# Kernel tuning notes

Measured on AMD Instinct MI355X. Metric: run time of the kernel, lower is better.

The kernel has to match this reference:

```python
import jax, jax.numpy as jnp
import numpy as np

BN_EPS = 1e-5

def _conv1x1(x, w, b=None):
    # x: [B,C,H,W], w: [O,C] -> [B,O,H,W]
    y = jnp.einsum('bchw,oc->bohw', x, w)
    if b is not None:
        y = y + b[None, :, None, None]
    return y

def _bn_silu(y, gamma, beta):
    # BN inference with running_mean=0, running_var=1, then SiLU
    scale = gamma / jnp.sqrt(1.0 + BN_EPS)
    y = y * scale[None, :, None, None] + beta[None, :, None, None]
    return jax.nn.silu(y)

def setup_inputs() -> dict:
    key = jax.random.key(0)
    ks = jax.random.split(key, 20)
    B, D, S = 32, 512, 32
    C = D // 2
    d = {}
    d['x'] = jax.random.normal(ks[0], (B, D, S, S), jnp.float32)
    d['cv1_w'] = jax.random.normal(ks[1], (C, D), jnp.float32) * (1.0 / np.sqrt(D))
    d['cv1_gamma'] = jax.random.uniform(ks[2], (C,), jnp.float32, 0.5, 1.5)
    d['cv1_beta'] = jax.random.normal(ks[3], (C,), jnp.float32) * 0.1
    d['q_w'] = jax.random.normal(ks[4], (C, C), jnp.float32) * (1.0 / np.sqrt(C))
    d['q_b'] = jax.random.normal(ks[5], (C,), jnp.float32) * 0.02
    d['k_w'] = jax.random.normal(ks[6], (C, C), jnp.float32) * (1.0 / np.sqrt(C))
    d['k_b'] = jax.random.normal(ks[7], (C,), jnp.float32) * 0.02
    d['v_w'] = jax.random.normal(ks[8], (C, C), jnp.float32) * (1.0 / np.sqrt(C))
    d['v_b'] = jax.random.normal(ks[9], (C,), jnp.float32) * 0.02
    d['e_w'] = jax.random.normal(ks[10], (C, C), jnp.float32) * (1.0 / np.sqrt(C))
    d['e_b'] = jax.random.normal(ks[11], (C,), jnp.float32) * 0.02
    d['rel_h'] = jax.random.normal(ks[12], (1, C, S, 1), jnp.float32)
    d['rel_w'] = jax.random.normal(ks[13], (1, C, 1, S), jnp.float32)
    d['cv2_w'] = jax.random.normal(ks[14], (D, C), jnp.float32) * (1.0 / np.sqrt(C))
    d['cv2_gamma'] = jax.random.uniform(ks[15], (D,), jnp.float32, 0.5, 1.5)
    d['cv2_beta'] = jax.random.normal(ks[16], (D,), jnp.float32) * 0.1
    return d

def reference(x, cv1_w, cv1_gamma, cv1_beta, q_w, q_b, k_w, k_b, v_w, v_b,
              e_w, e_b, rel_h, rel_w, cv2_w, cv2_gamma, cv2_beta):
    # cv1: 1x1 conv (no bias) + BN + SiLU
    x1 = _bn_silu(_conv1x1(x, cv1_w), cv1_gamma, cv1_beta)  # [B,C,H,W]
    B, C, H, W = x1.shape
    N = H * W
    q = _conv1x1(x1, q_w, q_b).reshape(B, C, N)
    k = _conv1x1(x1, k_w, k_b).reshape(B, C, N)
    v = _conv1x1(x1, v_w, v_b).reshape(B, C, N)
    e = _conv1x1(x1, e_w, e_b).reshape(B, C, N)
    # content-content: q^T k -> [B,N,N]
    cc = jnp.einsum('bci,bcj->bij', q, k)
    # content-position: (rel_h + rel_w) flattened to [C,N], times extra proj
    pos = (rel_h + rel_w).reshape(C, N)  # broadcast add -> [1,C,H,W] -> [C,N]
    cp = jnp.einsum('ci,bcj->bij', pos, e)  # [B,N,N]
    attn = jax.nn.softmax(cc + cp, axis=-1)
    # out[b,c,i] = sum_j v[b,c,j] * attn[b,i,j]
    out = jnp.einsum('bcj,bij->bci', v, attn).reshape(B, C, H, W)
    y = _bn_silu(_conv1x1(out, cv2_w), cv2_gamma, cv2_beta)
    return x + y
```

## Files before the change

### kernel.cpp

```cpp
#include <hip/hip_runtime.h>
#include <hip/hip_bf16.h>

typedef unsigned short u16;
typedef __attribute__((ext_vector_type(8))) _Float16 half8;
typedef __attribute__((ext_vector_type(4))) float f32x4;

__device__ __forceinline__ u16 f2h(float f) {
  _Float16 h = (_Float16)f;
  union { _Float16 h; u16 u; } a; a.h = h;
  return a.u;
}

__device__ __forceinline__ float h2f(u16 u) {
  union { _Float16 h; u16 u; } a; a.u = u;
  return (float)a.h;
}

__device__ __forceinline__ float silu_f(float y) {
  return y / (1.0f + __expf(-y));
}

__device__ __forceinline__ void glds16(const u16* g, u16* l) {
  __builtin_amdgcn_global_load_lds(
      (__attribute__((address_space(1))) unsigned*)(g),
      (__attribute__((address_space(3))) unsigned*)(l), 16, 0, 0);
}

enum { EPI_BNSILU_N = 0, EPI_QKEV, EPI_RAW_F16, EPI_BNSILU_RES_M };

template<int EPI, bool DUAL, int TILES, int GX>
__global__ __launch_bounds__(256, 2)
void gemm_nt(const u16* __restrict__ A, long long a_bs, int lda,
             const u16* __restrict__ A2,
             const u16* __restrict__ B, long long b_bs, int ldb,
             void* __restrict__ C0, long long c_bs, int ldc,
             void* __restrict__ C1, void* __restrict__ C2,
             int K,
             const float* __restrict__ p0, const float* __restrict__ p1,
             const float* __restrict__ res, long long res_bs)
{
  __shared__ u16 smem[8192];
  u16* lA = smem;
  u16* lB = smem + 4096;

  int bm, bn, bz;
  if constexpr (TILES > 0) {
    const int id = blockIdx.x;
    bz = (id & 7) + 8 * (id / (8 * TILES));
    const int tt = (id >> 3) % TILES;
    bm = tt % GX;
    bn = tt / GX;
  } else {
    bm = blockIdx.x; bn = blockIdx.y; bz = blockIdx.z;
  }
  const u16* Ab = A + (long long)bz * a_bs;
  const u16* Bb = B + (long long)bz * b_bs;
  const int m0 = bm * 128;
  const int n0 = bn * 128;
  const int t = threadIdx.x;
  const int lane = t & 63;
  const int w = t >> 6;
  const int wm = (w & 1) * 64;
  const int wn = (w >> 1) * 64;
  const int q = lane >> 4;
  const int lr = lane & 15;

  f32x4 acc[4][4];
#pragma unroll
  for (int i = 0; i < 4; ++i)
#pragma unroll
    for (int j = 0; j < 4; ++j)
      acc[i][j] = (f32x4){0.f, 0.f, 0.f, 0.f};

  const int lrow = lane >> 2;
  const int kch = (lane & 3) ^ ((lane >> 2) & 3) ^ ((lane >> 4) & 3);
  const int lk = kch * 8;
  const u16* aR0 = Ab + (long long)(m0 + 32 * w + lrow) * lda + lk;
  const u16* aR1 = aR0 + 16LL * lda;
  const u16* bR0 = Bb + (long long)(n0 + 32 * w + lrow) * ldb + lk;
  const u16* bR1 = bR0 + 16LL * ldb;
  const u16* a2R0 = nullptr; const u16* a2R1 = nullptr;
  if constexpr (DUAL) {
    a2R0 = A2 + (long long)(m0 + 32 * w + lrow) * 256 + lk;
    a2R1 = a2R0 + 16LL * 256;
  }
  u16* la0 = lA + w * 1024; u16* la1 = la0 + 512;
  u16* lb0 = lB + w * 1024; u16* lb1 = lb0 + 512;

  const int fpos = (q ^ (lr & 3) ^ ((lr >> 2) & 3)) * 8;

  for (int k0 = 0; k0 < K; k0 += 32) {
    __syncthreads();
    if (!DUAL || k0 < 256) {
      glds16(aR0 + k0, la0);
      glds16(aR1 + k0, la1);
    } else {
      glds16(a2R0 + (k0 - 256), la0);
      glds16(a2R1 + (k0 - 256), la1);
    }
    glds16(bR0 + k0, lb0);
    glds16(bR1 + k0, lb1);
    __syncthreads();
    half8 af[4], bfr[4];
#pragma unroll
    for (int i = 0; i < 4; ++i)
      af[i] = *(const half8*)&lA[(wm + i * 16 + lr) * 32 + fpos];
#pragma unroll
    for (int j = 0; j < 4; ++j)
      bfr[j] = *(const half8*)&lB[(wn + j * 16 + lr) * 32 + fpos];
#pragma unroll
    for (int i = 0; i < 4; ++i)
#pragma unroll
      for (int j = 0; j < 4; ++j)
        acc[i][j] = __builtin_amdgcn_mfma_f32_16x16x32_f16(af[i], bfr[j], acc[i][j], 0, 0, 0);
  }

  if constexpr (EPI == EPI_BNSILU_N) {
    u16* Cg = (u16*)C0 + (long long)bz * c_bs;
#pragma unroll
    for (int i = 0; i < 4; ++i)
#pragma unroll
      for (int j = 0; j < 4; ++j)
#pragma unroll
        for (int r = 0; r < 4; ++r) {
          const int m = m0 + wm + i * 16 + q * 4 + r;
          const int n = n0 + wn + j * 16 + lr;
          float v = acc[i][j][r];
          v = silu_f(v * (p0[n] * 0.99999500003749969f) + p1[n]);
          Cg[(long long)m * ldc + n] = f2h(v);
        }
  } else if constexpr (EPI == EPI_RAW_F16) {
    u16* Cg = (u16*)C0 + (long long)bz * c_bs;
#pragma unroll
    for (int i = 0; i < 4; ++i)
#pragma unroll
      for (int j = 0; j < 4; ++j)
#pragma unroll
        for (int r = 0; r < 4; ++r) {
          const int m = m0 + wm + i * 16 + q * 4 + r;
          const int n = n0 + wn + j * 16 + lr;
          Cg[(long long)m * ldc + n] = f2h(acc[i][j][r]);
        }
  } else if constexpr (EPI == EPI_BNSILU_RES_M) {
    float* Cg = (float*)C0 + (long long)bz * c_bs;
    const float* rg = res + (long long)bz * res_bs;
#pragma unroll
    for (int i = 0; i < 4; ++i)
#pragma unroll
      for (int j = 0; j < 4; ++j)
#pragma unroll
        for (int r = 0; r < 4; ++r) {
          const int m = m0 + wm + i * 16 + q * 4 + r;
          const int n = n0 + wn + j * 16 + lr;
          float v = acc[i][j][r];
          v = silu_f(v * (p0[m] * 0.99999500003749969f) + p1[m]);
          const long long idx = (long long)m * ldc + n;
          Cg[idx] = v + rg[idx];
        }
  } else {
    const int seg = n0 >> 8;
    const int nb = n0 & 255;
    if (seg < 3) {
      u16* dst; long long bs; int ld2;
      if (seg == 0) { dst = (u16*)C0; bs = 262144; ld2 = 256; }
      else { dst = (u16*)C1 + (seg == 2 ? 256 : 0); bs = 524288; ld2 = 512; }
      dst += (long long)bz * bs;
#pragma unroll
      for (int i = 0; i < 4; ++i)
#pragma unroll
        for (int j = 0; j < 4; ++j)
#pragma unroll
          for (int r = 0; r < 4; ++r) {
            const int m = m0 + wm + i * 16 + q * 4 + r;
            const int col = wn + j * 16 + lr;
            float v = acc[i][j][r] + p0[n0 + col];
            dst[(long long)m * ld2 + nb + col] = f2h(v);
          }
    } else {
      u16* dst = (u16*)C2 + (long long)bz * 262144;
#pragma unroll
      for (int s = 0; s < 4; ++s) {
        const int rbase = s * 32;
        __syncthreads();
        if (wm == (rbase & 64)) {
          const int ibase = (rbase & 32) >> 4;
#pragma unroll
          for (int ii = 0; ii < 2; ++ii) {
            const int i = ibase + ii;
#pragma unroll
            for (int j = 0; j < 4; ++j)
#pragma unroll
              for (int r = 0; r < 4; ++r) {
                const int row32 = i * 16 + q * 4 + r - (rbase & 32);
                const int col = wn + j * 16 + lr;
                float v = acc[i][j][r] + p0[768 + nb + col];
                smem[row32 * 132 + col] = f2h(v);
              }
          }
        }
        __syncthreads();
#pragma unroll
        for (int p = 0; p < 2; ++p) {
          const int lin = p * 256 + t;
          const int c = lin >> 2;
          const int mc = lin & 3;
          u16 tmp[8];
#pragma unroll
          for (int r8 = 0; r8 < 8; ++r8)
            tmp[r8] = smem[(mc * 8 + r8) * 132 + c];
          *(half8*)&dst[(long long)(nb + c) * 1024 + m0 + rbase + mc * 8] =
              *(const half8*)tmp;
        }
      }
    }
  }
}

__global__ __launch_bounds__(256)
void transpose_x(const float* __restrict__ x, u16* __restrict__ xT) {
  __shared__ float tile[64][33];
  const int b = blockIdx.z;
  const int n0 = blockIdx.x * 32;
  const int d0 = blockIdx.y * 64;
  const int tx = threadIdx.x;
  const int ty = threadIdx.y;
  const float* src = x + (long long)b * 524288;
#pragma unroll
  for (int i = 0; i < 8; ++i)
    tile[ty + 8 * i][tx] = src[(long long)(d0 + ty + 8 * i) * 1024 + n0 + tx];
  __syncthreads();
  u16* dst = xT + (long long)b * 524288;
#pragma unroll
  for (int i = 0; i < 4; ++i) {
    const int n = ty + 8 * i;
    unsigned lo = (unsigned)f2h(tile[2 * tx][n]);
    unsigned hi = (unsigned)f2h(tile[2 * tx + 1][n]);
    *(unsigned*)&dst[(long long)(n0 + n) * 512 + d0 + 2 * tx] = lo | (hi << 16);
  }
}

__global__ __launch_bounds__(256)
void convert_w(const float* __restrict__ w1, const float* __restrict__ wq,
               const float* __restrict__ wk, const float* __restrict__ wv,
               const float* __restrict__ we, const float* __restrict__ w2,
               const float* __restrict__ bq, const float* __restrict__ bk,
               const float* __restrict__ be, const float* __restrict__ bv,
               u16* __restrict__ dstw, float* __restrict__ bbuf) {
  int id = blockIdx.x * 256 + threadIdx.x;
  if (id < 524288) {
    float v;
    if (id < 131072) v = w1[id];
    else if (id < 393216) {
      int s = id - 131072, o = s >> 8, c = s & 255;
      if (o < 256) v = wq[o * 256 + c];
      else if (o < 512) v = wk[(o - 256) * 256 + c];
      else if (o < 768) v = we[(o - 512) * 256 + c];
      else v = wv[(o - 768) * 256 + c];
    } else v = w2[id - 393216];
    dstw[id] = f2h(v);
  } else {
    int i = id - 524288;
    float v;
    if (i < 256) v = bq[i];
    else if (i < 512) v = bk[i - 256];
    else if (i < 768) v = be[i - 512];
    else v = bv[i - 768];
    bbuf[i] = v;
  }
}

__global__ __launch_bounds__(256)
void pos_compute(const float* __restrict__ rh, const float* __restrict__ rw,
                 u16* __restrict__ posT) {
  const int n = blockIdx.x;
  const int c = threadIdx.x;
  posT[n * 256 + c] = f2h(rh[c * 32 + (n >> 5)] + rw[c * 32 + (n & 31)]);
}

__global__ __launch_bounds__(256)
void softmax_rows(u16* __restrict__ logits) {
  __shared__ float red[8];
  u16* p = logits + (long long)blockIdx.x * 1024;
  const int t = threadIdx.x;
  ushort4 raw = ((const ushort4*)p)[t];
  float v0 = h2f(raw.x), v1 = h2f(raw.y), v2 = h2f(raw.z), v3 = h2f(raw.w);
  float mx = fmaxf(fmaxf(v0, v1), fmaxf(v2, v3));
#pragma unroll
  for (int off = 32; off > 0; off >>= 1) mx = fmaxf(mx, __shfl_down(mx, off));
  const int lane = t & 63, w = t >> 6;
  if (lane == 0) red[w] = mx;
  __syncthreads();
  mx = fmaxf(fmaxf(red[0], red[1]), fmaxf(red[2], red[3]));
  float e0 = __expf(v0 - mx), e1 = __expf(v1 - mx),
        e2 = __expf(v2 - mx), e3 = __expf(v3 - mx);
  float s = e0 + e1 + e2 + e3;
#pragma unroll
  for (int off = 32; off > 0; off >>= 1) s += __shfl_down(s, off);
  if (lane == 0) red[4 + w] = s;
  __syncthreads();
  const float inv = 1.0f / (red[4] + red[5] + red[6] + red[7]);
  ushort4 o;
  o.x = f2h(e0 * inv); o.y = f2h(e1 * inv); o.z = f2h(e2 * inv); o.w = f2h(e3 * inv);
  ((ushort4*)p)[t] = o;
}

extern "C" void kernel_launch(void* const* d_in, const int* in_sizes, int n_in,
                              void* d_out, int out_size, void* d_ws, size_t ws_size,
                              hipStream_t stream) {
  const float* x  = (const float*)d_in[0];
  const float* w1 = (const float*)d_in[1];
  const float* g1 = (const float*)d_in[2];
  const float* b1 = (const float*)d_in[3];
  const float* wq = (const float*)d_in[4];
  const float* bq = (const float*)d_in[5];
  const float* wk = (const float*)d_in[6];
  const float* bk = (const float*)d_in[7];
  const float* wv = (const float*)d_in[8];
  const float* bv = (const float*)d_in[9];
  const float* we = (const float*)d_in[10];
  const float* be = (const float*)d_in[11];
  const float* rh = (const float*)d_in[12];
  const float* rw = (const float*)d_in[13];
  const float* w2 = (const float*)d_in[14];
  const float* g2 = (const float*)d_in[15];
  const float* b2 = (const float*)d_in[16];
  float* out = (float*)d_out;
  char* ws = (char*)d_ws;

  u16* xT     = (u16*)(ws + 0);
  u16* x1t    = (u16*)(ws + 33554432);
  u16* qbuf   = (u16*)(ws + 50331648);
  u16* kcat   = (u16*)(ws + 67108864);
  u16* vbuf   = (u16*)(ws + 100663296);
  u16* outt   = (u16*)(ws + 117440512);
  u16* posT   = (u16*)(ws + 134217728);
  u16* wbuf   = (u16*)(ws + 134742016);
  float* bbuf = (float*)(ws + 135790592);
  u16* logits = (u16*)(ws + 142606336);

  u16* w1b    = wbuf;
  u16* wqkve  = wbuf + 131072;
  u16* w2b    = wbuf + 393216;

  transpose_x<<<dim3(32, 8, 32), dim3(32, 8), 0, stream>>>(x, xT);
  convert_w<<<dim3(2052), 256, 0, stream>>>(w1, wq, wk, wv, we, w2,
                                            bq, bk, be, bv, wbuf, bbuf);
  pos_compute<<<dim3(1024), 256, 0, stream>>>(rh, rw, posT);

  gemm_nt<EPI_BNSILU_N, false, 16, 8><<<dim3(512), 256, 0, stream>>>(
      xT, 524288LL, 512, nullptr, w1b, 0LL, 512,
      x1t, 262144LL, 256, nullptr, nullptr, 512, g1, b1, nullptr, 0LL);

  gemm_nt<EPI_QKEV, false, 64, 8><<<dim3(2048), 256, 0, stream>>>(
      x1t, 262144LL, 256, nullptr, wqkve, 0LL, 256,
      qbuf, 262144LL, 256, kcat, vbuf, 256, bbuf, nullptr, nullptr, 0LL);

  gemm_nt<EPI_RAW_F16, true, 64, 8><<<dim3(2048), 256, 0, stream>>>(
      qbuf, 262144LL, 256, posT, kcat, 524288LL, 512,
      logits, 1048576LL, 1024, nullptr, nullptr, 512, nullptr, nullptr, nullptr, 0LL);

  softmax_rows<<<dim3(32768), 256, 0, stream>>>(logits);

  gemm_nt<EPI_RAW_F16, false, 16, 8><<<dim3(512), 256, 0, stream>>>(
      logits, 1048576LL, 1024, nullptr, vbuf, 262144LL, 1024,
      outt, 262144LL, 256, nullptr, nullptr, 1024, nullptr, nullptr, nullptr, 0LL);

  gemm_nt<EPI_BNSILU_RES_M, false, 32, 4><<<dim3(1024), 256, 0, stream>>>(
      w2b, 0LL, 256, nullptr, outt, 262144LL, 256,
      out, 524288LL, 1024, nullptr, nullptr, 256, g2, b2, x, 524288LL);
}
```

Baseline: 341.3 us.

## Fuse softmax into PV GEMM using row max from logits epilogue atomics

The logits GEMM epilogue now reduces each row's partial max and publishes it with an atomicMax on order-preserving encoded floats. The separate softmax pass is removed, and a new pv_softmax kernel computes exp2 of the raw logits against that row max on the fly. It feeds the exponentials straight into the MFMA A operand and normalizes by the accumulated row sum in the epilogue. This drops one full read-write pass over the large fp16 logits buffer. In exchange it adds global atomics, exp work repeated for each of the two N-tiles, and uncached direct global A loads instead of LDS staging.

```diff
diff --git a/kernel.cpp b/kernel.cpp
--- a/kernel.cpp
+++ b/kernel.cpp
@@ -4,6 +4,8 @@
 typedef unsigned short u16;
 typedef __attribute__((ext_vector_type(8))) _Float16 half8;
 typedef __attribute__((ext_vector_type(4))) float f32x4;
+
+#define LOG2E 1.44269504088896340736f
 
 __device__ __forceinline__ u16 f2h(float f) {
   _Float16 h = (_Float16)f;
@@ -20,13 +22,22 @@
   return y / (1.0f + __expf(-y));
 }
 
+__device__ __forceinline__ unsigned fenc(float f) {
+  unsigned b = __float_as_uint(f);
+  return (b & 0x80000000u) ? ~b : (b | 0x80000000u);
+}
+__device__ __forceinline__ float fdec(unsigned u) {
+  unsigned b = (u & 0x80000000u) ? (u ^ 0x80000000u) : ~u;
+  return __uint_as_float(b);
+}
+
 __device__ __forceinline__ void glds16(const u16* g, u16* l) {
   __builtin_amdgcn_global_load_lds(
       (__attribute__((address_space(1))) unsigned*)(g),
       (__attribute__((address_space(3))) unsigned*)(l), 16, 0, 0);
 }
 
-enum { EPI_BNSILU_N = 0, EPI_QKEV, EPI_RAW_F16, EPI_BNSILU_RES_M };
+enum { EPI_BNSILU_N = 0, EPI_QKEV, EPI_RAW_F16, EPI_LOGITS, EPI_BNSILU_RES_M };
 
 template<int EPI, bool DUAL, int TILES, int GX>
 __global__ __launch_bounds__(256, 2)
@@ -37,22 +48,18 @@
              void* __restrict__ C1, void* __restrict__ C2,
              int K,
              const float* __restrict__ p0, const float* __restrict__ p1,
-             const float* __restrict__ res, long long res_bs)
+             const float* __restrict__ res, long long res_bs,
+             unsigned* __restrict__ rmax)
 {
   __shared__ u16 smem[8192];
   u16* lA = smem;
   u16* lB = smem + 4096;
 
-  int bm, bn, bz;
-  if constexpr (TILES > 0) {
-    const int id = blockIdx.x;
-    bz = (id & 7) + 8 * (id / (8 * TILES));
-    const int tt = (id >> 3) % TILES;
-    bm = tt % GX;
-    bn = tt / GX;
-  } else {
-    bm = blockIdx.x; bn = blockIdx.y; bz = blockIdx.z;
-  }
+  const int id = blockIdx.x;
+  const int bz = (id & 7) + 8 * (id / (8 * TILES));
+  const int tt = (id >> 3) % TILES;
+  const int bm = tt % GX;
+  const int bn = tt / GX;
   const u16* Ab = A + (long long)bz * a_bs;
   const u16* Bb = B + (long long)bz * b_bs;
   const int m0 = bm * 128;
@@ -86,7 +93,6 @@
   }
   u16* la0 = lA + w * 1024; u16* la1 = la0 + 512;
   u16* lb0 = lB + w * 1024; u16* lb1 = lb0 + 512;
-
   const int fpos = (q ^ (lr & 3) ^ ((lr >> 2) & 3)) * 8;
 
   for (int k0 = 0; k0 < K; k0 += 32) {
@@ -129,7 +135,7 @@
           v = silu_f(v * (p0[n] * 0.99999500003749969f) + p1[n]);
           Cg[(long long)m * ldc + n] = f2h(v);
         }
-  } else if constexpr (EPI == EPI_RAW_F16) {
+  } else if constexpr (EPI == EPI_RAW_F16 || EPI == EPI_LOGITS) {
     u16* Cg = (u16*)C0 + (long long)bz * c_bs;
 #pragma unroll
     for (int i = 0; i < 4; ++i)
@@ -141,6 +147,21 @@
           const int n = n0 + wn + j * 16 + lr;
           Cg[(long long)m * ldc + n] = f2h(acc[i][j][r]);
         }
+    if constexpr (EPI == EPI_LOGITS) {
+#pragma unroll
+      for (int i = 0; i < 4; ++i)
+#pragma unroll
+        for (int r = 0; r < 4; ++r) {
+          float mx = fmaxf(fmaxf(acc[i][0][r], acc[i][1][r]),
+                           fmaxf(acc[i][2][r], acc[i][3][r]));
+          mx = fmaxf(mx, __shfl_xor(mx, 1));
+          mx = fmaxf(mx, __shfl_xor(mx, 2));
+          mx = fmaxf(mx, __shfl_xor(mx, 4));
+          mx = fmaxf(mx, __shfl_xor(mx, 8));
+          if (lr == 0)
+            atomicMax(&rmax[bz * 1024 + m0 + wm + i * 16 + q * 4 + r], fenc(mx));
+        }
+    }
   } else if constexpr (EPI == EPI_BNSILU_RES_M) {
     float* Cg = (float*)C0 + (long long)bz * c_bs;
     const float* rg = res + (long long)bz * res_bs;
@@ -214,6 +235,105 @@
       }
     }
   }
+}
+
+__global__ __launch_bounds__(256, 2)
+void pv_softmax(const u16* __restrict__ P, const unsigned* __restrict__ rmaxu,
+                const u16* __restrict__ V, u16* __restrict__ O) {
+  __shared__ u16 smem[4096];
+  const int id = blockIdx.x;
+  const int bz = (id & 7) + 8 * (id / 128);
+  const int tt = (id >> 3) & 15;
+  const int m0 = (tt & 7) * 128;
+  const int n0 = (tt >> 3) * 128;
+  const int t = threadIdx.x;
+  const int lane = t & 63;
+  const int w = t >> 6;
+  const int wm = (w & 1) * 64;
+  const int wn = (w >> 1) * 64;
+  const int q = lane >> 4;
+  const int lr = lane & 15;
+
+  f32x4 acc[4][4];
+#pragma unroll
+  for (int i = 0; i < 4; ++i)
+#pragma unroll
+    for (int j = 0; j < 4; ++j)
+      acc[i][j] = (f32x4){0.f, 0.f, 0.f, 0.f};
+
+  const int lrow = lane >> 2;
+  const int kch = (lane & 3) ^ ((lane >> 2) & 3) ^ ((lane >> 4) & 3);
+  const int lk = kch * 8;
+  const u16* bR0 = V + (long long)bz * 262144 +
+                   (long long)(n0 + 32 * w + lrow) * 1024 + lk;
+  const u16* bR1 = bR0 + 16 * 1024;
+  u16* lb0 = smem + w * 1024; u16* lb1 = lb0 + 512;
+  const int fpos = (q ^ (lr & 3) ^ ((lr >> 2) & 3)) * 8;
+
+  const u16* Ab = P + (long long)bz * 1048576;
+  const u16* pA[4];
+  float ml[4], lsum[4];
+#pragma unroll
+  for (int i = 0; i < 4; ++i) {
+    const int row = m0 + wm + i * 16 + lr;
+    pA[i] = Ab + (long long)row * 1024 + q * 8;
+    ml[i] = fdec(rmaxu[bz * 1024 + row]) * LOG2E;
+    lsum[i] = 0.f;
+  }
+
+  for (int k0 = 0; k0 < 1024; k0 += 32) {
+    __syncthreads();
+    glds16(bR0 + k0, lb0);
+    glds16(bR1 + k0, lb1);
+    half8 paf[4];
+#pragma unroll
+    for (int i = 0; i < 4; ++i) {
+      half8 raw = *(const half8*)(pA[i] + k0);
+      float e[8];
+#pragma unroll
+      for (int u = 0; u < 8; ++u)
+        e[u] = exp2f(fmaf((float)raw[u], LOG2E, -ml[i]));
+      lsum[i] += ((e[0] + e[1]) + (e[2] + e[3])) + ((e[4] + e[5]) + (e[6] + e[7]));
+#pragma unroll
+      for (int u = 0; u < 8; ++u) paf[i][u] = (_Float16)e[u];
+    }
+    __syncthreads();
+    half8 bfr[4];
+#pragma unroll
+    for (int j = 0; j < 4; ++j)
+      bfr[j] = *(const half8*)&smem[(wn + j * 16 + lr) * 32 + fpos];
+#pragma unroll
+    for (int i = 0; i < 4; ++i)
+#pragma unroll
+      for (int j = 0; j < 4; ++j)
+        acc[i][j] = __builtin_amdgcn_mfma_f32_16x16x32_f16(paf[i], bfr[j], acc[i][j], 0, 0, 0);
+  }
+
+#pragma unroll
+  for (int i = 0; i < 4; ++i) {
+    lsum[i] += __shfl_xor(lsum[i], 16);
+    lsum[i] += __shfl_xor(lsum[i], 32);
+  }
+  __syncthreads();
+  float* rowl = (float*)smem;
+  if (lane < 16) {
+#pragma unroll
+    for (int i = 0; i < 4; ++i)
+      rowl[wm + i * 16 + lane] = lsum[i];
+  }
+  __syncthreads();
+  u16* Og = O + (long long)bz * 262144;
+#pragma unroll
+  for (int i = 0; i < 4; ++i)
+#pragma unroll
+    for (int r = 0; r < 4; ++r) {
+      const int row = wm + i * 16 + q * 4 + r;
+      const float inv = 1.0f / rowl[row];
+#pragma unroll
+      for (int j = 0; j < 4; ++j)
+        Og[(long long)(m0 + row) * 256 + n0 + wn + j * 16 + lr] =
+            f2h(acc[i][j][r] * inv);
+    }
 }
 
 __global__ __launch_bounds__(256)
@@ -271,37 +391,12 @@
 
 __global__ __launch_bounds__(256)
 void pos_compute(const float* __restrict__ rh, const float* __restrict__ rw,
-                 u16* __restrict__ posT) {
+                 u16* __restrict__ posT, unsigned* __restrict__ rmaxu) {
   const int n = blockIdx.x;
   const int c = threadIdx.x;
   posT[n * 256 + c] = f2h(rh[c * 32 + (n >> 5)] + rw[c * 32 + (n & 31)]);
-}
-
-__global__ __launch_bounds__(256)
-void softmax_rows(u16* __restrict__ logits) {
-  __shared__ float red[8];
-  u16* p = logits + (long long)blockIdx.x * 1024;
-  const int t = threadIdx.x;
-  ushort4 raw = ((const ushort4*)p)[t];
-  float v0 = h2f(raw.x), v1 = h2f(raw.y), v2 = h2f(raw.z), v3 = h2f(raw.w);
-  float mx = fmaxf(fmaxf(v0, v1), fmaxf(v2, v3));
-#pragma unroll
-  for (int off = 32; off > 0; off >>= 1) mx = fmaxf(mx, __shfl_down(mx, off));
-  const int lane = t & 63, w = t >> 6;
-  if (lane == 0) red[w] = mx;
-  __syncthreads();
-  mx = fmaxf(fmaxf(red[0], red[1]), fmaxf(red[2], red[3]));
-  float e0 = __expf(v0 - mx), e1 = __expf(v1 - mx),
-        e2 = __expf(v2 - mx), e3 = __expf(v3 - mx);
-  float s = e0 + e1 + e2 + e3;
-#pragma unroll
-  for (int off = 32; off > 0; off >>= 1) s += __shfl_down(s, off);
-  if (lane == 0) red[4 + w] = s;
-  __syncthreads();
-  const float inv = 1.0f / (red[4] + red[5] + red[6] + red[7]);
-  ushort4 o;
-  o.x = f2h(e0 * inv); o.y = f2h(e1 * inv); o.z = f2h(e2 * inv); o.w = f2h(e3 * inv);
-  ((ushort4*)p)[t] = o;
+  const int idx = n * 256 + c;
+  if (idx < 32768) rmaxu[idx] = 0x007fffffu;
 }
 
 extern "C" void kernel_launch(void* const* d_in, const int* in_sizes, int n_in,
@@ -327,16 +422,17 @@
   float* out = (float*)d_out;
   char* ws = (char*)d_ws;
 
-  u16* xT     = (u16*)(ws + 0);
-  u16* x1t    = (u16*)(ws + 33554432);
-  u16* qbuf   = (u16*)(ws + 50331648);
-  u16* kcat   = (u16*)(ws + 67108864);
-  u16* vbuf   = (u16*)(ws + 100663296);
-  u16* outt   = (u16*)(ws + 117440512);
-  u16* posT   = (u16*)(ws + 134217728);
-  u16* wbuf   = (u16*)(ws + 134742016);
-  float* bbuf = (float*)(ws + 135790592);
-  u16* logits = (u16*)(ws + 142606336);
+  u16* xT       = (u16*)(ws + 0);
+  u16* x1t      = (u16*)(ws + 33554432);
+  u16* qbuf     = (u16*)(ws + 50331648);
+  u16* kcat     = (u16*)(ws + 67108864);
+  u16* vbuf     = (u16*)(ws + 100663296);
+  u16* outt     = (u16*)(ws + 117440512);
+  u16* posT     = (u16*)(ws + 134217728);
+  u16* wbuf     = (u16*)(ws + 134742016);
+  float* bbuf   = (float*)(ws + 135790592);
+  unsigned* rmx = (unsigned*)(ws + 136314880);
+  u16* logits   = (u16*)(ws + 142606336);
 
   u16* w1b    = wbuf;
   u16* wqkve  = wbuf + 131072;
@@ -345,27 +441,23 @@
   transpose_x<<<dim3(32, 8, 32), dim3(32, 8), 0, stream>>>(x, xT);
   convert_w<<<dim3(2052), 256, 0, stream>>>(w1, wq, wk, wv, we, w2,
                                             bq, bk, be, bv, wbuf, bbuf);
-  pos_compute<<<dim3(1024), 256, 0, stream>>>(rh, rw, posT);
+  pos_compute<<<dim3(1024), 256, 0, stream>>>(rh, rw, posT, rmx);
 
   gemm_nt<EPI_BNSILU_N, false, 16, 8><<<dim3(512), 256, 0, stream>>>(
       xT, 524288LL, 512, nullptr, w1b, 0LL, 512,
-      x1t, 262144LL, 256, nullptr, nullptr, 512, g1, b1, nullptr, 0LL);
+      x1t, 262144LL, 256, nullptr, nullptr, 512, g1, b1, nullptr, 0LL, nullptr);
 
   gemm_nt<EPI_QKEV, false, 64, 8><<<dim3(2048), 256, 0, stream>>>(
       x1t, 262144LL, 256, nullptr, wqkve, 0LL, 256,
-      qbuf, 262144LL, 256, kcat, vbuf, 256, bbuf, nullptr, nullptr, 0LL);
-
-  gemm_nt<EPI_RAW_F16, true, 64, 8><<<dim3(2048), 256, 0, stream>>>(
+      qbuf, 262144LL, 256, kcat, vbuf, 256, bbuf, nullptr, nullptr, 0LL, nullptr);
+
+  gemm_nt<EPI_LOGITS, true, 64, 8><<<dim3(2048), 256, 0, stream>>>(
       qbuf, 262144LL, 256, posT, kcat, 524288LL, 512,
-      logits, 1048576LL, 1024, nullptr, nullptr, 512, nullptr, nullptr, nullptr, 0LL);
-
-  softmax_rows<<<dim3(32768), 256, 0, stream>>>(logits);
-
-  gemm_nt<EPI_RAW_F16, false, 16, 8><<<dim3(512), 256, 0, stream>>>(
-      logits, 1048576LL, 1024, nullptr, vbuf, 262144LL, 1024,
-      outt, 262144LL, 256, nullptr, nullptr, 1024, nullptr, nullptr, nullptr, 0LL);
+      logits, 1048576LL, 1024, nullptr, nullptr, 512, nullptr, nullptr, nullptr, 0LL, rmx);
+
+  pv_softmax<<<dim3(512), 256, 0, stream>>>(logits, rmx, vbuf, outt);
 
   gemm_nt<EPI_BNSILU_RES_M, false, 32, 4><<<dim3(1024), 256, 0, stream>>>(
       w2b, 0LL, 256, nullptr, outt, 262144LL, 256,
-      out, 524288LL, 1024, nullptr, nullptr, 256, g2, b2, x, 524288LL);
-}
+      out, 524288LL, 1024, nullptr, nullptr, 256, g2, b2, x, 524288LL, nullptr);
+}
```

Measured after the change: 363.4 us. 1.06x slower.
